# Optimization experiments

Measured on AMD Instinct MI355X. Metric: run time of the kernel, lower is better.

Reference implementation:

```python
import jax, jax.numpy as jnp
import numpy as np

Q_EPS = 1e-12  # scale clamp used in from_float


def _quantize_rows(w):
    # per-row symmetric int8 quantization: scale = absmax/127, clamp 1e-12
    scales = jnp.clip(jnp.max(jnp.abs(w), axis=1) / 127.0, Q_EPS, None)  # [rows]
    w_i8 = jnp.clip(jnp.round(w / scales[:, None]), -128.0, 127.0)       # int values, fp32 carrier
    return w_i8, scales


def setup_inputs() -> dict:
    key = jax.random.key(0)
    k1, k2, k3 = jax.random.split(key, 3)
    B, S, K, N = 2, 4096, 4096, 4096
    x = jax.random.normal(k1, (B, S, K), dtype=jnp.float32)
    weight_fp = jax.random.normal(k2, (N, K), dtype=jnp.float32) * 0.02
    bias = jax.random.normal(k3, (N,), dtype=jnp.float32) * 0.01
    return {"x": x, "weight_fp": weight_fp, "bias": bias}


def reference(x, weight_fp, bias):
    orig_dtype = x.dtype
    # weight quantization (from_float): per-output-channel scales
    w_i8, w_scales = _quantize_rows(weight_fp)          # [N,K], [N]
    # per-token dynamic activation quantization
    x_shape = x.shape
    x_flat = x.reshape(-1, x_shape[-1])                 # [M,K]
    x_i8, x_scales = _quantize_rows(x_flat)             # [M,K], [M]
    # int8 GEMM accumulated exactly (values fit fp32), fused dequant
    acc = jnp.matmul(x_i8, w_i8.T)                      # [M,N] integer-valued
    out = acc * x_scales[:, None] * w_scales[None, :]
    out = out.astype(jnp.bfloat16)                      # kernel outputs bf16
    out = out.reshape(*x_shape[:-1], w_i8.shape[0])
    out = out + bias.astype(out.dtype)
    return out.astype(orig_dtype)
```

## Files before the change

kernel.cpp:

```cpp
#include <hip/hip_runtime.h>
#include <hip/hip_bf16.h>
#include <stdint.h>


using i32x4  = __attribute__((ext_vector_type(4))) int;
using i32x16 = __attribute__((ext_vector_type(16))) int;

#define TILE 128
#define BK 64

__global__ __launch_bounds__(256) void quant_rows_fused(
    const float* __restrict__ w_in, const float* __restrict__ x_in,
    int8_t* __restrict__ w_q, int8_t* __restrict__ x_q,
    float* __restrict__ w_s, float* __restrict__ x_s,
    int nw, int K)
{
    const int b   = blockIdx.x;
    const bool is_w = (b < nw);
    const int row = is_w ? b : (b - nw);
    const float* r = (is_w ? w_in : x_in) + (size_t)row * K;
    int8_t* qout   = (is_w ? w_q : x_q) + (size_t)row * K;
    float* scales  = is_w ? w_s : x_s;

    const int tid = threadIdx.x;

    float4 v[4];
#pragma unroll
    for (int j = 0; j < 4; ++j)
        v[j] = *(const float4*)(r + j * 1024 + tid * 4);

    float amax = 0.f;
#pragma unroll
    for (int j = 0; j < 4; ++j) {
        amax = fmaxf(amax, fabsf(v[j].x));
        amax = fmaxf(amax, fabsf(v[j].y));
        amax = fmaxf(amax, fabsf(v[j].z));
        amax = fmaxf(amax, fabsf(v[j].w));
    }

#pragma unroll
    for (int off = 32; off >= 1; off >>= 1)
        amax = fmaxf(amax, __shfl_xor(amax, off));

    __shared__ float red[4];
    const int wave = tid >> 6;
    if ((tid & 63) == 0) red[wave] = amax;
    __syncthreads();
    amax = fmaxf(fmaxf(red[0], red[1]), fmaxf(red[2], red[3]));

    const float scale = fmaxf(amax / 127.0f, 1e-12f);
    if (tid == 0) scales[row] = scale;

#pragma unroll
    for (int j = 0; j < 4; ++j) {
        float q0 = fminf(fmaxf(rintf(v[j].x / scale), -128.f), 127.f);
        float q1 = fminf(fmaxf(rintf(v[j].y / scale), -128.f), 127.f);
        float q2 = fminf(fmaxf(rintf(v[j].z / scale), -128.f), 127.f);
        float q3 = fminf(fmaxf(rintf(v[j].w / scale), -128.f), 127.f);
        union { signed char c[4]; int i; } u;
        u.c[0] = (signed char)(int)q0;
        u.c[1] = (signed char)(int)q1;
        u.c[2] = (signed char)(int)q2;
        u.c[3] = (signed char)(int)q3;
        *(int*)(qout + j * 1024 + tid * 4) = u.i;
    }
}

__global__ __launch_bounds__(256) void gemm_i8_kernel(
    const int8_t* __restrict__ A,
    const int8_t* __restrict__ B,
    const float*  __restrict__ xs,
    const float*  __restrict__ ws,
    const float*  __restrict__ bias,
    float*        __restrict__ out,
    int M, int N, int K)
{
    __shared__ int8_t sA[TILE * BK];
    __shared__ int8_t sB[TILE * BK];

    const int tid   = threadIdx.x;
    const int wave  = tid >> 6;
    const int lane  = tid & 63;
    const int l31   = lane & 31;
    const int lhalf = lane >> 5;

    const int bm = blockIdx.y * TILE;
    const int bn = blockIdx.x * TILE;
    const int wm = (wave >> 1) * 64;
    const int wn = (wave & 1) * 64;

    i32x16 acc[2][2];
#pragma unroll
    for (int i = 0; i < 2; ++i)
#pragma unroll
        for (int j = 0; j < 2; ++j)
#pragma unroll
            for (int r = 0; r < 16; ++r) acc[i][j][r] = 0;

    const int srow = tid >> 2;
    const int g    = ((tid & 3) - ((tid >> 3) & 3)) & 3;
    const int soff = g * 16;

    const int8_t* aptr0 = A + (size_t)(bm + srow) * K + soff;
    const int8_t* aptr1 = A + (size_t)(bm + 64 + srow) * K + soff;
    const int8_t* bptr0 = B + (size_t)(bn + srow) * K + soff;
    const int8_t* bptr1 = B + (size_t)(bn + 64 + srow) * K + soff;

    int8_t* sA0 = sA + tid * 16;
    int8_t* sA1 = sA + 4096 + tid * 16;
    int8_t* sB0 = sB + tid * 16;
    int8_t* sB1 = sB + 4096 + tid * 16;

    const int pc0 = ((lhalf + 0 + (l31 >> 1)) & 3) * 16;
    const int pc1 = ((lhalf + 2 + (l31 >> 1)) & 3) * 16;

    for (int k0 = 0; k0 < K; k0 += BK) {
        __syncthreads();
        __builtin_amdgcn_global_load_lds(
            (const __attribute__((address_space(1))) void*)(aptr0 + k0),
            (__attribute__((address_space(3))) void*)sA0, 16, 0, 0);
        __builtin_amdgcn_global_load_lds(
            (const __attribute__((address_space(1))) void*)(aptr1 + k0),
            (__attribute__((address_space(3))) void*)sA1, 16, 0, 0);
        __builtin_amdgcn_global_load_lds(
            (const __attribute__((address_space(1))) void*)(bptr0 + k0),
            (__attribute__((address_space(3))) void*)sB0, 16, 0, 0);
        __builtin_amdgcn_global_load_lds(
            (const __attribute__((address_space(1))) void*)(bptr1 + k0),
            (__attribute__((address_space(3))) void*)sB1, 16, 0, 0);
        __syncthreads();

        i32x4 af[2][2], bf[2][2];
#pragma unroll
        for (int it = 0; it < 2; ++it) {
            const int arow = (wm + it * 32 + l31) * BK;
            af[it][0] = *(const i32x4*)(sA + arow + pc0);
            af[it][1] = *(const i32x4*)(sA + arow + pc1);
        }
#pragma unroll
        for (int jt = 0; jt < 2; ++jt) {
            const int brow = (wn + jt * 32 + l31) * BK;
            bf[jt][0] = *(const i32x4*)(sB + brow + pc0);
            bf[jt][1] = *(const i32x4*)(sB + brow + pc1);
        }

#pragma unroll
        for (int kh = 0; kh < 2; ++kh)
#pragma unroll
            for (int it = 0; it < 2; ++it)
#pragma unroll
                for (int jt = 0; jt < 2; ++jt)
                    acc[it][jt] = __builtin_amdgcn_mfma_i32_32x32x32_i8(
                        af[it][kh], bf[jt][kh], acc[it][jt], 0, 0, 0);
    }

#pragma unroll
    for (int jt = 0; jt < 2; ++jt) {
        const int col = bn + wn + jt * 32 + l31;
        const float wsv = ws[col];
        const float bsv = __bfloat162float(__float2bfloat16(bias[col]));
#pragma unroll
        for (int it = 0; it < 2; ++it) {
            const int rowbase = bm + wm + it * 32 + 4 * lhalf;
#pragma unroll
            for (int r = 0; r < 16; ++r) {
                const int row = rowbase + (r & 3) + 8 * (r >> 2);
                const float v = (float)acc[it][jt][r] * xs[row] * wsv;
                const float vb = __bfloat162float(__float2bfloat16(v));
                const float res = __bfloat162float(__float2bfloat16(vb + bsv));
                out[(size_t)row * N + col] = res;
            }
        }
    }
}

extern "C" void kernel_launch(void* const* d_in, const int* in_sizes, int n_in,
                              void* d_out, int out_size, void* d_ws, size_t ws_size,
                              hipStream_t stream)
{
    const float* x    = (const float*)d_in[0];
    const float* wfp  = (const float*)d_in[1];
    const float* bias = (const float*)d_in[2];
    float* out = (float*)d_out;

    const int N = in_sizes[2];
    const int K = in_sizes[1] / N;
    const int M = in_sizes[0] / K;

    int8_t* w_i8 = (int8_t*)d_ws;
    int8_t* x_i8 = w_i8 + (size_t)N * K;
    float* w_scales = (float*)(x_i8 + (size_t)M * K);
    float* x_scales = w_scales + N;

    quant_rows_fused<<<N + M, 256, 0, stream>>>(wfp, x, w_i8, x_i8,
                                                w_scales, x_scales, N, K);

    dim3 grid(N / TILE, M / TILE);
    gemm_i8_kernel<<<grid, 256, 0, stream>>>(x_i8, w_i8, x_scales, w_scales,
                                             bias, out, M, N, K);
}
```

Baseline: 441.9 us.

## Double-buffer GEMM LDS tiles with register-staged prefetch of next K slice

Replaces the direct global-to-LDS loads with register-staged global loads of the next K tile, issued before the MFMAs on the current tile and written into the alternate LDS buffer afterwards. This cuts the loop to one barrier per iteration and lets global latency overlap compute. In exchange it doubles LDS usage and adds VGPR pressure for the staged registers. It also does one redundant wraparound load on the last iteration.

```diff
diff --git a/kernel.cpp b/kernel.cpp
--- a/kernel.cpp
+++ b/kernel.cpp
@@ -75,8 +75,7 @@
     float*        __restrict__ out,
     int M, int N, int K)
 {
-    __shared__ int8_t sA[TILE * BK];
-    __shared__ int8_t sB[TILE * BK];
+    __shared__ __align__(16) int8_t sAB[2][2 * TILE * BK];
 
     const int tid   = threadIdx.x;
     const int wave  = tid >> 6;
@@ -97,51 +96,58 @@
 #pragma unroll
             for (int r = 0; r < 16; ++r) acc[i][j][r] = 0;
 
-    const int srow = tid >> 2;
-    const int g    = ((tid & 3) - ((tid >> 3) & 3)) & 3;
-    const int soff = g * 16;
-
-    const int8_t* aptr0 = A + (size_t)(bm + srow) * K + soff;
-    const int8_t* aptr1 = A + (size_t)(bm + 64 + srow) * K + soff;
-    const int8_t* bptr0 = B + (size_t)(bn + srow) * K + soff;
-    const int8_t* bptr1 = B + (size_t)(bn + 64 + srow) * K + soff;
-
-    int8_t* sA0 = sA + tid * 16;
-    int8_t* sA1 = sA + 4096 + tid * 16;
-    int8_t* sB0 = sB + tid * 16;
-    int8_t* sB1 = sB + 4096 + tid * 16;
+    const int srow   = tid >> 2;
+    const int schunk = tid & 3;
+    const int wchunk = ((schunk + ((srow >> 1) & 3)) & 3) * 16;
+
+    const int8_t* ag0 = A + (size_t)(bm + srow) * K + schunk * 16;
+    const int8_t* ag1 = A + (size_t)(bm + 64 + srow) * K + schunk * 16;
+    const int8_t* bg0 = B + (size_t)(bn + srow) * K + schunk * 16;
+    const int8_t* bg1 = B + (size_t)(bn + 64 + srow) * K + schunk * 16;
+
+    const int wA0 = srow * 64 + wchunk;
+    const int wA1 = (srow + 64) * 64 + wchunk;
+    const int wB0 = 8192 + srow * 64 + wchunk;
+    const int wB1 = 8192 + (srow + 64) * 64 + wchunk;
 
     const int pc0 = ((lhalf + 0 + (l31 >> 1)) & 3) * 16;
     const int pc1 = ((lhalf + 2 + (l31 >> 1)) & 3) * 16;
 
-    for (int k0 = 0; k0 < K; k0 += BK) {
+    {
+        i32x4 ra0 = *(const i32x4*)(ag0);
+        i32x4 ra1 = *(const i32x4*)(ag1);
+        i32x4 rb0 = *(const i32x4*)(bg0);
+        i32x4 rb1 = *(const i32x4*)(bg1);
+        int8_t* wb = sAB[0];
+        *(i32x4*)(wb + wA0) = ra0;
+        *(i32x4*)(wb + wA1) = ra1;
+        *(i32x4*)(wb + wB0) = rb0;
+        *(i32x4*)(wb + wB1) = rb1;
+    }
+
+    int buf = 0;
+    for (int k0 = 0; k0 < K; k0 += BK, buf ^= 1) {
         __syncthreads();
-        __builtin_amdgcn_global_load_lds(
-            (const __attribute__((address_space(1))) void*)(aptr0 + k0),
-            (__attribute__((address_space(3))) void*)sA0, 16, 0, 0);
-        __builtin_amdgcn_global_load_lds(
-            (const __attribute__((address_space(1))) void*)(aptr1 + k0),
-            (__attribute__((address_space(3))) void*)sA1, 16, 0, 0);
-        __builtin_amdgcn_global_load_lds(
-            (const __attribute__((address_space(1))) void*)(bptr0 + k0),
-            (__attribute__((address_space(3))) void*)sB0, 16, 0, 0);
-        __builtin_amdgcn_global_load_lds(
-            (const __attribute__((address_space(1))) void*)(bptr1 + k0),
-            (__attribute__((address_space(3))) void*)sB1, 16, 0, 0);
-        __syncthreads();
-
-        i32x4 af[2][2], bf[2][2];
+
+        const int kn = (k0 + BK < K) ? (k0 + BK) : 0;
+        i32x4 ra0 = *(const i32x4*)(ag0 + kn);
+        i32x4 ra1 = *(const i32x4*)(ag1 + kn);
+        i32x4 rb0 = *(const i32x4*)(bg0 + kn);
+        i32x4 rb1 = *(const i32x4*)(bg1 + kn);
+
+        const int8_t* rb = sAB[buf];
+        i32x4 af[2][2], bfr[2][2];
 #pragma unroll
         for (int it = 0; it < 2; ++it) {
-            const int arow = (wm + it * 32 + l31) * BK;
-            af[it][0] = *(const i32x4*)(sA + arow + pc0);
-            af[it][1] = *(const i32x4*)(sA + arow + pc1);
+            const int arow = (wm + it * 32 + l31) * 64;
+            af[it][0] = *(const i32x4*)(rb + arow + pc0);
+            af[it][1] = *(const i32x4*)(rb + arow + pc1);
         }
 #pragma unroll
         for (int jt = 0; jt < 2; ++jt) {
-            const int brow = (wn + jt * 32 + l31) * BK;
-            bf[jt][0] = *(const i32x4*)(sB + brow + pc0);
-            bf[jt][1] = *(const i32x4*)(sB + brow + pc1);
+            const int brow = 8192 + (wn + jt * 32 + l31) * 64;
+            bfr[jt][0] = *(const i32x4*)(rb + brow + pc0);
+            bfr[jt][1] = *(const i32x4*)(rb + brow + pc1);
         }
 
 #pragma unroll
@@ -151,7 +157,13 @@
 #pragma unroll
                 for (int jt = 0; jt < 2; ++jt)
                     acc[it][jt] = __builtin_amdgcn_mfma_i32_32x32x32_i8(
-                        af[it][kh], bf[jt][kh], acc[it][jt], 0, 0, 0);
+                        af[it][kh], bfr[jt][kh], acc[it][jt], 0, 0, 0);
+
+        int8_t* wb = sAB[buf ^ 1];
+        *(i32x4*)(wb + wA0) = ra0;
+        *(i32x4*)(wb + wA1) = ra1;
+        *(i32x4*)(wb + wB0) = rb0;
+        *(i32x4*)(wb + wB1) = rb1;
     }
 
 #pragma unroll
```

Result: no change. 449.2 us (+1.6%).
